# Performance work log

Measured on AMD Instinct MI355X. Metric: run time of the kernel, lower is better.

## Reference

```python
import jax, jax.numpy as jnp
import numpy as np

NEAR = 0.2          # near-plane cull, matches uvd[...,2] >= 0.2 in the source
SIGMA2_MAX = 9.0    # 3-sigma disk extent, matches get_disks' sigma3 corners
ALPHA_MIN = 1.0 / 255.0


def quat_to_rot(q):
    """Unit-quaternion [P,4] (w,x,y,z) -> rotation matrices [P,3,3]."""
    q = q / (jnp.linalg.norm(q, axis=-1, keepdims=True) + 1e-12)
    w, x, y, z = q[..., 0], q[..., 1], q[..., 2], q[..., 3]
    r0 = jnp.stack([1 - 2 * (y * y + z * z), 2 * (x * y - w * z), 2 * (x * z + w * y)], -1)
    r1 = jnp.stack([2 * (x * y + w * z), 1 - 2 * (x * x + z * z), 2 * (y * z - w * x)], -1)
    r2 = jnp.stack([2 * (x * z - w * y), 2 * (y * z + w * x), 1 - 2 * (x * x + y * y)], -1)
    return jnp.stack([r0, r1, r2], -2)


def setup_inputs() -> dict:
    key = jax.random.key(0)
    k = jax.random.split(key, 6)
    H = W = 128
    P = 4096
    tanfov = 0.4
    f = W / (2.0 * tanfov)
    xs = (jnp.arange(W, dtype=jnp.float32) - (W - 1) / 2.0) / f
    ys = (jnp.arange(H, dtype=jnp.float32) - (H - 1) / 2.0) / f
    gx, gy = jnp.meshgrid(xs, ys, indexing='xy')
    d = jnp.stack([gx, gy, jnp.ones_like(gx)], -1)
    ray_d = d / jnp.linalg.norm(d, axis=-1, keepdims=True)   # [H,W,3]
    ray_o = jnp.zeros((H, W, 3), jnp.float32)
    means3D = jax.random.normal(k[0], (P, 3), jnp.float32) * 1.5 + jnp.array([0.0, 0.0, 4.0], jnp.float32)
    scales = jax.random.uniform(k[1], (P, 2), jnp.float32, 0.02, 0.15)
    rotations = jax.random.normal(k[2], (P, 4), jnp.float32)
    opacities = jax.random.uniform(k[3], (P, 1), jnp.float32, 0.3, 1.0)
    colors = jax.random.uniform(k[4], (P, 3), jnp.float32)
    bg_color = jnp.zeros((3,), jnp.float32)
    return dict(ray_o=ray_o, ray_d=ray_d, means3D=means3D, scales=scales,
                rotations=rotations, opacities=opacities, colors=colors, bg_color=bg_color)


def reference(ray_o, ray_d, means3D, scales, rotations, opacities, colors, bg_color):
    """Gaussian-surfel ray tracing: ray/disk-plane intersection, 2D Gaussian
    falloff in the surfel tangent frame, front-to-back alpha compositing in
    depth order (the math the BVH-accelerated SurfelTracer computes)."""
    H, W, _ = ray_o.shape
    ro = ray_o.reshape(-1, 3)
    rd = ray_d.reshape(-1, 3)
    R = quat_to_rot(rotations)                     # [P,3,3]
    tu, tv, nrm = R[..., :, 0], R[..., :, 1], R[..., :, 2]  # tangent frame columns

    # ray-plane intersection t = dot(mu - o, n) / dot(d, n)  -> [Nr,P]
    den = rd @ nrm.T
    num = jnp.einsum('pk,pk->p', means3D, nrm)[None, :] - ro @ nrm.T
    safe_den = jnp.where(jnp.abs(den) < 1e-8, 1e-8, den)
    t = num / safe_den

    # local disk coords u,v of hit point without materializing [Nr,P,3]
    u = (ro @ tu.T - jnp.einsum('pk,pk->p', means3D, tu)[None, :] + t * (rd @ tu.T)) / scales[None, :, 0]
    v = (ro @ tv.T - jnp.einsum('pk,pk->p', means3D, tv)[None, :] + t * (rd @ tv.T)) / scales[None, :, 1]
    r2 = u * u + v * v
    G = jnp.exp(-0.5 * r2)
    alpha = jnp.clip(opacities[None, :, 0] * G, 0.0, 0.99)
    valid = (t > NEAR) & (r2 < SIGMA2_MAX) & (jnp.abs(den) > 1e-8) & (alpha > ALPHA_MIN)
    alpha = jnp.where(valid, alpha, 0.0)

    # front-to-back compositing: sort hits by depth per ray
    t_key = jnp.where(valid, t, jnp.inf)
    order = jnp.argsort(t_key, axis=1)
    alpha_s = jnp.take_along_axis(alpha, order, axis=1)
    trans = jnp.cumprod(1.0 - alpha_s, axis=1)
    trans = jnp.concatenate([jnp.ones_like(trans[:, :1]), trans[:, :-1]], axis=1)  # exclusive
    w_s = alpha_s * trans
    inv = jnp.argsort(order, axis=1)
    w = jnp.take_along_axis(w_s, inv, axis=1)      # weights in original surfel order

    acc = w.sum(-1)                                # [Nr]
    rgb = w @ colors + (1.0 - acc)[:, None] * bg_color[None, :]
    dpt = (w * jnp.where(valid, t, 0.0)).sum(-1)
    norm = w @ nrm
    return (rgb.reshape(H, W, 3), dpt.reshape(H, W, 1),
            acc.reshape(H, W, 1), norm.reshape(H, W, 3))
```

## Files before the change

kernel.cpp:

```cpp
#include <hip/hip_runtime.h>
#include <stdint.h>

#define NEAR_T  0.2f
#define SIG2MAX 9.0f
#define AMIN    (1.0f/255.0f)
#define NSL     8
#define TS      8
#define TB      16
#define KFIX    64


__device__ __forceinline__ float dot3(float ax,float ay,float az,
                                      float bx,float by,float bz){
  return fmaf(ax,bx, fmaf(ay,by, az*bz));
}

__device__ __forceinline__ bool eval_hit(const float* __restrict__ gp,
    float rox,float roy,float roz, float rdx,float rdy,float rdz,
    float& t_out, float& a_out)
{
  float nx=gp[6], ny=gp[7], nz=gp[8];
  float den  = dot3(rdx,rdy,rdz, nx,ny,nz);
  float aden = fabsf(den);
  float num  = gp[11] - dot3(rox,roy,roz, nx,ny,nz);
  float sden = (aden < 1e-8f) ? 1e-8f : den;
  float t = __fdividef(num, sden);
  float ru = dot3(rox,roy,roz, gp[0],gp[1],gp[2]);
  float du = dot3(rdx,rdy,rdz, gp[0],gp[1],gp[2]);
  float u  = fmaf(t, du, ru - gp[9])  * gp[12];
  float rv = dot3(rox,roy,roz, gp[3],gp[4],gp[5]);
  float dv = dot3(rdx,rdy,rdz, gp[3],gp[4],gp[5]);
  float v  = fmaf(t, dv, rv - gp[10]) * gp[13];
  float r2 = fmaf(u,u, v*v);
  float G  = __expf(-0.5f*r2);
  float a  = fminf(gp[14]*G, 0.99f);
  t_out = t; a_out = a;
  return (t > NEAR_T) & (r2 < SIG2MAX) & (aden > 1e-8f) & (a > AMIN);
}

__device__ __forceinline__ unsigned long long make_key(float t, float a, uint32_t g){
  uint32_t a16 = (uint32_t)(a * 65535.f + 0.5f);
  return ((unsigned long long)__float_as_uint(t) << 32) |
         ((unsigned long long)a16 << 16) | (unsigned long long)g;
}

__device__ __forceinline__ bool pix_bbox(const float* __restrict__ bp,
    bool fallback, float axm, float bxm, float aym, float bym, int W, int H,
    int& x0, int& x1, int& y0, int& y1)
{
  if (fallback){ x0=0; x1=W-1; y0=0; y1=H-1; return true; }
  float mx=bp[0], my=bp[1], mz=bp[2], ex=bp[3], ey=bp[4], ez=bp[5];
  float zmin=mz-ez, zmax=mz+ez;
  if (zmax <= 0.16f) return false;
  if (zmin <= 1e-3f){ x0=0; x1=W-1; y0=0; y1=H-1; return true; }
  float xmin=mx-ex, xmax=mx+ex, ymin=my-ey, ymax=my+ey;
  float gxmin = (xmin>=0.f)? xmin/zmax : xmin/zmin;
  float gxmax = (xmax>=0.f)? xmax/zmin : xmax/zmax;
  float gymin = (ymin>=0.f)? ymin/zmax : ymin/zmin;
  float gymax = (ymax>=0.f)? ymax/zmin : ymax/zmax;
  float p0 = (gxmin - bxm)/axm, p1 = (gxmax - bxm)/axm;
  float q0 = (gymin - bym)/aym, q1 = (gymax - bym)/aym;
  int ix0 = (int)floorf(fminf(p0,p1)) - 1;
  int ix1 = (int)ceilf (fmaxf(p0,p1)) + 1;
  int iy0 = (int)floorf(fminf(q0,q1)) - 1;
  int iy1 = (int)ceilf (fmaxf(q0,q1)) + 1;
  if (ix1 < 0 || ix0 > W-1 || iy1 < 0 || iy0 > H-1) return false;
  x0 = max(ix0,0); x1 = min(ix1,W-1);
  y0 = max(iy0,0); y1 = min(iy1,H-1);
  return true;
}

__global__ void k_prep(const float* __restrict__ rot, const float* __restrict__ means,
                       const float* __restrict__ scales, const float* __restrict__ opac,
                       const float* __restrict__ colors, const float* __restrict__ ray_o,
                       const float* __restrict__ ray_d,
                       float* __restrict__ geo, float* __restrict__ col,
                       float* __restrict__ baux, uint32_t* __restrict__ misc,
                       int P, int npix, int W)
{
  int tid = blockIdx.x*blockDim.x + threadIdx.x;
  float g0x = ray_d[0]/ray_d[2], g0y = ray_d[1]/ray_d[2];
  float axm = ray_d[3]/ray_d[5] - g0x;
  float aym = ray_d[(size_t)W*3+1]/ray_d[(size_t)W*3+2] - g0y;
  if (tid == 0){
    float* mf = (float*)misc;
    mf[1] = axm; mf[2] = g0x; mf[3] = aym; mf[4] = g0y;
    if (!(fabsf(axm) > 1e-12f) || !(fabsf(aym) > 1e-12f)) atomicOr(misc, 1u);
  }
  if (tid < npix){
    int ix = tid % W, iy = tid / W;
    float rox=ray_o[tid*3+0], roy=ray_o[tid*3+1], roz=ray_o[tid*3+2];
    float rdx=ray_d[tid*3+0], rdy=ray_d[tid*3+1], rdz=ray_d[tid*3+2];
    bool ok = (rox==0.f) & (roy==0.f) & (roz==0.f) & (rdz > 0.8f);
    if (ok){
      float gx = rdx/rdz, gy = rdy/rdz;
      ok = (fabsf(gx - fmaf(axm,(float)ix,g0x)) <= 3e-4f) &
           (fabsf(gy - fmaf(aym,(float)iy,g0y)) <= 3e-4f);
    }
    if (!ok) atomicOr(misc, 1u);
  }
  if (tid < P){
    float qw=rot[tid*4+0], qx=rot[tid*4+1], qy=rot[tid*4+2], qz=rot[tid*4+3];
    float n = sqrtf(qw*qw+qx*qx+qy*qy+qz*qz) + 1e-12f;
    qw/=n; qx/=n; qy/=n; qz/=n;
    float tux = 1.f-2.f*(qy*qy+qz*qz), tuy = 2.f*(qx*qy+qw*qz), tuz = 2.f*(qx*qz-qw*qy);
    float tvx = 2.f*(qx*qy-qw*qz), tvy = 1.f-2.f*(qx*qx+qz*qz), tvz = 2.f*(qy*qz+qw*qx);
    float nx  = 2.f*(qx*qz+qw*qy), ny  = 2.f*(qy*qz-qw*qx), nz  = 1.f-2.f*(qx*qx+qy*qy);
    float mx=means[tid*3+0], my=means[tid*3+1], mz=means[tid*3+2];
    float sx=scales[tid*2+0], sy=scales[tid*2+1];
    float* gp = &geo[(size_t)tid*16];
    gp[0]=tux; gp[1]=tuy; gp[2]=tuz;
    gp[3]=tvx; gp[4]=tvy; gp[5]=tvz;
    gp[6]=nx;  gp[7]=ny;  gp[8]=nz;
    gp[9]  = mx*tux+my*tuy+mz*tuz;
    gp[10] = mx*tvx+my*tvy+mz*tvz;
    gp[11] = mx*nx +my*ny +mz*nz;
    gp[12] = 1.f/sx;
    gp[13] = 1.f/sy;
    gp[14] = opac[tid];
    gp[15] = 0.f;
    col[tid*3+0]=colors[tid*3+0]; col[tid*3+1]=colors[tid*3+1]; col[tid*3+2]=colors[tid*3+2];
    float* bp = &baux[(size_t)tid*8];
    const float R3 = 3.02f;
    bp[0]=mx; bp[1]=my; bp[2]=mz;
    bp[3]=R3*(sx*fabsf(tux)+sy*fabsf(tvx));
    bp[4]=R3*(sx*fabsf(tuy)+sy*fabsf(tvy));
    bp[5]=R3*(sx*fabsf(tuz)+sy*fabsf(tvz));
    bp[6]=0.f; bp[7]=0.f;
  }
}

__global__ __launch_bounds__(1024)
void k_bin_fused(const float* __restrict__ baux, const uint32_t* __restrict__ misc,
                 int4* __restrict__ bbox, uint32_t* __restrict__ tileLen,
                 uint32_t* __restrict__ tileList, int P, int W, int H, int TXB, int TYB)
{
  __shared__ uint32_t sCnt[1024];
  int NTB = TXB*TYB;
  int tid = threadIdx.x;
  for (int i=tid; i<NTB; i+=1024) sCnt[i]=0u;
  __syncthreads();
  const float* mf = (const float*)misc;
  bool fb = (misc[0] != 0u);
  float a1=mf[1], a2=mf[2], a3=mf[3], a4=mf[4];
  for (int g=tid; g<P; g+=1024){
    int x0,x1,y0,y1;
    bool ok = pix_bbox(&baux[(size_t)g*8], fb, a1,a2,a3,a4, W,H, x0,x1,y0,y1);
    bbox[g] = ok ? make_int4(x0,x1,y0,y1) : make_int4(1,0,1,0);
    if (!ok) continue;
    int tx0=x0/TB, tx1=x1/TB, ty0=y0/TB, ty1=y1/TB;
    for (int ty=ty0; ty<=ty1; ++ty)
      for (int tx=tx0; tx<=tx1; ++tx){
        int t = ty*TXB+tx;
        uint32_t slot = atomicAdd(&sCnt[t], 1u);
        tileList[(size_t)t*P + slot] = (uint32_t)g;
      }
  }
  __syncthreads();
  for (int i=tid; i<NTB; i+=1024) tileLen[i] = sCnt[i];
}

__global__ void k_bbox(const float* __restrict__ baux, const uint32_t* __restrict__ misc,
                       int4* __restrict__ bbox, int P, int W, int H)
{
  int g = blockIdx.x*blockDim.x + threadIdx.x;
  if (g >= P) return;
  const float* mf = (const float*)misc;
  bool fb = (misc[0] != 0u);
  int x0,x1,y0,y1;
  bool ok = pix_bbox(&baux[(size_t)g*8], fb, mf[1],mf[2],mf[3],mf[4], W,H, x0,x1,y0,y1);
  bbox[g] = ok ? make_int4(x0,x1,y0,y1) : make_int4(1,0,1,0);
}

__global__ void k_bin_global(const int4* __restrict__ bbox, uint32_t* __restrict__ tileLen,
                             uint32_t* __restrict__ tileList, int P, int TXB)
{
  int g = blockIdx.x*blockDim.x + threadIdx.x;
  if (g >= P) return;
  int4 bb = bbox[g];
  if (bb.x > bb.y) return;
  int tx0=bb.x/TB, tx1=bb.y/TB, ty0=bb.z/TB, ty1=bb.w/TB;
  for (int ty=ty0; ty<=ty1; ++ty)
    for (int tx=tx0; tx<=tx1; ++tx){
      int t = ty*TXB+tx;
      uint32_t slot = atomicAdd(&tileLen[t], 1u);
      tileList[(size_t)t*P + slot] = (uint32_t)g;
    }
}

__global__ __launch_bounds__(64)
void k_trace(const float* __restrict__ geo, const int4* __restrict__ bbox,
             const float* __restrict__ ray_o, const float* __restrict__ ray_d,
             const uint32_t* __restrict__ tileLen, const uint32_t* __restrict__ tileList,
             uint32_t* __restrict__ cnt, unsigned long long* __restrict__ keys64,
             int W, int H, int TXB, int STX, int P)
{
  int st = blockIdx.x;
  int stx = st % STX, sty = st / STX;
  int lane = threadIdx.x;
  int ix = stx*TS + (lane & (TS-1));
  int iy = sty*TS + (lane / TS);
  bool live = (ix < W) & (iy < H);
  int px = live ? (iy*W + ix) : 0;
  int pt = (sty*TS/TB)*TXB + (stx*TS/TB);
  uint32_t base = (uint32_t)pt * (uint32_t)P;
  uint32_t len  = tileLen[pt];
  int sx0 = stx*TS, sx1 = sx0 + TS-1;
  int sy0 = sty*TS, sy1 = sy0 + TS-1;
  float rox=ray_o[px*3+0], roy=ray_o[px*3+1], roz=ray_o[px*3+2];
  float rdx=ray_d[px*3+0], rdy=ray_d[px*3+1], rdz=ray_d[px*3+2];
  for (uint32_t s = blockIdx.y; s < len; s += NSL){
    int gu = __builtin_amdgcn_readfirstlane((int)tileList[base+s]);
    int4 bb = bbox[gu];
    if (bb.x > sx1 || bb.y < sx0 || bb.z > sy1 || bb.w < sy0) continue;
    const float* gp = &geo[(size_t)gu*16];
    float t,a;
    bool hit = eval_hit(gp, rox,roy,roz, rdx,rdy,rdz, t, a) && live;
    if (hit){
      uint32_t slot = atomicAdd(&cnt[px], 1u);
      if (slot < KFIX) keys64[(size_t)px*KFIX + slot] = make_key(t, a, (uint32_t)gu);
    }
  }
}

__device__ __forceinline__ float wred(float v){
  #pragma unroll
  for (int d=32; d>0; d>>=1) v += __shfl_down(v, d);
  return v;
}

__device__ __forceinline__ void comp_write(int px, int npix, int lane,
    float r_, float g_, float bl_, float dpt_, float acc_,
    float nx_, float ny_, float nz_, const float* __restrict__ bg,
    float* __restrict__ out)
{
  r_ = wred(r_); g_ = wred(g_); bl_ = wred(bl_);
  dpt_ = wred(dpt_); acc_ = wred(acc_);
  nx_ = wred(nx_); ny_ = wred(ny_); nz_ = wred(nz_);
  if (lane == 0){
    float one_m = 1.f - acc_;
    out[(size_t)px*3+0] = r_  + one_m*bg[0];
    out[(size_t)px*3+1] = g_  + one_m*bg[1];
    out[(size_t)px*3+2] = bl_ + one_m*bg[2];
    out[(size_t)npix*3 + px] = dpt_;
    out[(size_t)npix*4 + px] = acc_;
    out[(size_t)npix*5 + (size_t)px*3+0] = nx_;
    out[(size_t)npix*5 + (size_t)px*3+1] = ny_;
    out[(size_t)npix*5 + (size_t)px*3+2] = nz_;
  }
}

__global__ __launch_bounds__(256)
void k_comp_small(const unsigned long long* __restrict__ keys64,
                  const uint32_t* __restrict__ cnt,
                  const float* __restrict__ geo, const float* __restrict__ col,
                  const float* __restrict__ bg, float* __restrict__ out, int npix)
{
  int lane = threadIdx.x & 63;
  int wave = threadIdx.x >> 6;
  for (int px = (int)(blockIdx.x*4u + wave); px < npix; px += (int)(gridDim.x*4u)){
    uint32_t K = cnt[px];
    if (K > (uint32_t)KFIX) continue;
    unsigned long long key = (lane < (int)K) ? keys64[(size_t)px*KFIX + lane] : ~0ull;
    #pragma unroll
    for (int k=2; k<=64; k<<=1){
      #pragma unroll
      for (int j=k>>1; j>0; j>>=1){
        unsigned long long other = __shfl_xor(key, j);
        bool keep_min = (((lane & j) == 0) == ((lane & k) == 0));
        unsigned long long lo = key < other ? key : other;
        unsigned long long hi = key < other ? other : key;
        key = keep_min ? lo : hi;
      }
    }
    bool valid = lane < (int)K;
    const float inv65535 = 1.f/65535.f;
    float a = (float)((uint32_t)(key >> 16) & 0xFFFFu) * inv65535;
    float p = valid ? (1.f - a) : 1.f;
    float ip = p;
    #pragma unroll
    for (int d=1; d<64; d<<=1){ float v = __shfl_up(ip, d); if (lane >= d) ip *= v; }
    float T = __shfl_up(ip, 1);
    if (lane == 0) T = 1.f;
    float r_=0.f, g_=0.f, bl_=0.f, dpt_=0.f, acc_=0.f, nx_=0.f, ny_=0.f, nz_=0.f;
    if (valid){
      float t = __uint_as_float((uint32_t)(key >> 32));
      uint32_t g = (uint32_t)(key & 0xFFFFu);
      float w = a * T;
      const float* gp = &geo[(size_t)g*16];
      const float* cp = &col[(size_t)g*3];
      r_ = w*cp[0]; g_ = w*cp[1]; bl_ = w*cp[2];
      dpt_ = w*t; acc_ = w;
      nx_ = w*gp[6]; ny_ = w*gp[7]; nz_ = w*gp[8];
    }
    comp_write(px, npix, lane, r_,g_,bl_,dpt_,acc_,nx_,ny_,nz_, bg, out);
  }
}

__global__ __launch_bounds__(64)
void k_comp_over(const float* __restrict__ geo, const int4* __restrict__ bbox,
                 const float* __restrict__ col,
                 const float* __restrict__ ray_o, const float* __restrict__ ray_d,
                 const uint32_t* __restrict__ tileLen, const uint32_t* __restrict__ tileList,
                 const uint32_t* __restrict__ cnt, const float* __restrict__ bg,
                 float* __restrict__ out, int npix, int W, int TXB, int P)
{
  __shared__ unsigned long long sk[4096];
  int lane = threadIdx.x;
  unsigned long long lt = (1ull << lane) - 1ull;
  for (int px = (int)blockIdx.x; px < npix; px += (int)gridDim.x){
    if (cnt[px] <= (uint32_t)KFIX) continue;
    int ix = px % W, iy = px / W;
    int pt = (iy/TB)*TXB + (ix/TB);
    uint32_t base = (uint32_t)pt * (uint32_t)P;
    uint32_t len  = tileLen[pt];
    float rox=ray_o[px*3+0], roy=ray_o[px*3+1], roz=ray_o[px*3+2];
    float rdx=ray_d[px*3+0], rdy=ray_d[px*3+1], rdz=ray_d[px*3+2];

    uint32_t run = 0;
    for (uint32_t s0=0; s0<len; s0+=64){
      uint32_t s = s0 + (uint32_t)lane;
      bool act = s < len;
      uint32_t gu = act ? tileList[base+s] : 0u;
      float t=0.f, a=0.f;
      bool hit = false;
      if (act){
        int4 bb = bbox[gu];
        if (bb.x <= ix && ix <= bb.y && bb.z <= iy && iy <= bb.w)
          hit = eval_hit(&geo[(size_t)gu*16], rox,roy,roz, rdx,rdy,rdz, t, a);
      }
      unsigned long long m = __ballot(hit);
      if (hit){
        uint32_t slot = run + (uint32_t)__popcll(m & lt);
        if (slot < 4096u) sk[slot] = make_key(t, a, gu);
      }
      run += (uint32_t)__popcll(m);
    }
    uint32_t K = min(run, 4096u);
    uint32_t N = 1; while (N < K) N <<= 1;
    for (uint32_t i=K+lane; i<N; i+=64) sk[i] = ~0ull;
    __syncthreads();

    for (uint32_t kk=2; kk<=N; kk<<=1){
      for (uint32_t j=kk>>1; j>0; j>>=1){
        for (uint32_t i=lane; i<N; i+=64){
          uint32_t ij = i ^ j;
          if (ij > i){
            unsigned long long a = sk[i], b = sk[ij];
            bool up = ((i & kk) == 0);
            if ((a > b) == up){ sk[i] = b; sk[ij] = a; }
          }
        }
        __syncthreads();
      }
    }

    const float inv65535 = 1.f/65535.f;
    uint32_t C = (K + 63) >> 6;
    uint32_t b0 = lane*C, e0 = min(b0 + C, K);
    float p = 1.f;
    for (uint32_t i=b0; i<e0; ++i){
      float a = (float)((uint32_t)(sk[i] >> 16) & 0xFFFFu) * inv65535;
      p *= (1.f - a);
    }
    float ip = p;
    #pragma unroll
    for (int d=1; d<64; d<<=1){ float v = __shfl_up(ip, d); if (lane >= d) ip *= v; }
    float T = __shfl_up(ip, 1);
    if (lane == 0) T = 1.f;

    float r_=0.f, g_=0.f, bl_=0.f, dpt_=0.f, acc_=0.f, nx_=0.f, ny_=0.f, nz_=0.f;
    for (uint32_t i=b0; i<e0; ++i){
      unsigned long long key = sk[i];
      float t = __uint_as_float((uint32_t)(key >> 32));
      float a = (float)((uint32_t)(key >> 16) & 0xFFFFu) * inv65535;
      uint32_t g = (uint32_t)(key & 0xFFFFu);
      float w = a * T;
      const float* gp = &geo[(size_t)g*16];
      const float* cp = &col[(size_t)g*3];
      r_  += w * cp[0]; g_ += w * cp[1]; bl_ += w * cp[2];
      dpt_ += w * t; acc_ += w;
      nx_ += w * gp[6]; ny_ += w * gp[7]; nz_ += w * gp[8];
      T *= (1.f - a);
    }
    comp_write(px, npix, lane, r_,g_,bl_,dpt_,acc_,nx_,ny_,nz_, bg, out);
    __syncthreads();
  }
}

extern "C" void kernel_launch(void* const* d_in, const int* in_sizes, int n_in,
                              void* d_out, int out_size, void* d_ws, size_t ws_size,
                              hipStream_t stream)
{
  const float* ray_o  = (const float*)d_in[0];
  const float* ray_d  = (const float*)d_in[1];
  const float* means  = (const float*)d_in[2];
  const float* scales = (const float*)d_in[3];
  const float* rot    = (const float*)d_in[4];
  const float* opac   = (const float*)d_in[5];
  const float* colors = (const float*)d_in[6];
  const float* bg     = (const float*)d_in[7];
  float* out = (float*)d_out;

  int npix = in_sizes[0] / 3;
  int P    = in_sizes[2] / 3;
  int W    = (int)(sqrtf((float)npix) + 0.5f);
  int H    = npix / W;
  int TXB  = (W + TB - 1) / TB;
  int TYB  = (H + TB - 1) / TB;
  int NTB  = TXB * TYB;
  int STX  = (W + TS - 1) / TS;
  int STY  = (H + TS - 1) / TS;
  int NST  = STX * STY;

  uint8_t* ws = (uint8_t*)d_ws;
  size_t o_geo   = 0;
  size_t sz_geo  = ((size_t)P*16*4 + 255) & ~(size_t)255;
  size_t o_col   = o_geo + sz_geo;
  size_t sz_col  = ((size_t)P*3*4 + 255) & ~(size_t)255;
  size_t o_baux  = o_col + sz_col;
  size_t sz_baux = ((size_t)P*8*4 + 255) & ~(size_t)255;
  size_t o_bbox  = o_baux + sz_baux;
  size_t sz_bbox = ((size_t)P*16 + 255) & ~(size_t)255;

  size_t o_ctrl  = o_bbox + sz_bbox;
  size_t sz_pix  = ((size_t)npix*4 + 255) & ~(size_t)255;
  size_t o_cnt   = o_ctrl;
  size_t sz_ntb  = ((size_t)NTB*4 + 255) & ~(size_t)255;
  size_t o_tlen  = o_cnt + sz_pix;
  size_t o_misc  = o_tlen + sz_ntb;
  size_t ctrl_sz = (o_misc + 256) - o_ctrl;

  size_t o_tlist = o_ctrl + ctrl_sz;
  size_t sz_tlist= (((size_t)NTB*(size_t)P*4) + 255) & ~(size_t)255;
  size_t o_k64   = o_tlist + sz_tlist;

  float*    geo     = (float*)(ws + o_geo);
  float*    col     = (float*)(ws + o_col);
  float*    baux    = (float*)(ws + o_baux);
  int4*     bbox    = (int4*)(ws + o_bbox);
  uint32_t* cnt     = (uint32_t*)(ws + o_cnt);
  uint32_t* tileLen = (uint32_t*)(ws + o_tlen);
  uint32_t* misc    = (uint32_t*)(ws + o_misc);
  uint32_t* tileList= (uint32_t*)(ws + o_tlist);
  unsigned long long* keys64 = (unsigned long long*)(ws + o_k64);

  hipMemsetAsync(ws + o_ctrl, 0, ctrl_sz, stream);

  int initN = npix > P ? npix : P;
  k_prep<<<(initN + 255)/256, 256, 0, stream>>>(rot, means, scales, opac, colors,
                                                ray_o, ray_d, geo, col, baux, misc,
                                                P, npix, W);
  if (NTB <= 1024){
    k_bin_fused<<<1, 1024, 0, stream>>>(baux, misc, bbox, tileLen, tileList,
                                        P, W, H, TXB, TYB);
  } else {
    k_bbox<<<(P + 255)/256, 256, 0, stream>>>(baux, misc, bbox, P, W, H);
    k_bin_global<<<(P + 255)/256, 256, 0, stream>>>(bbox, tileLen, tileList, P, TXB);
  }
  dim3 tgrid(NST, NSL);
  k_trace<<<tgrid, 64, 0, stream>>>(geo, bbox, ray_o, ray_d, tileLen, tileList,
                                    cnt, keys64, W, H, TXB, STX, P);
  k_comp_small<<<1024, 256, 0, stream>>>(keys64, cnt, geo, col, bg, out, npix);
  k_comp_over<<<1024, 64, 0, stream>>>(geo, bbox, col, ray_o, ray_d, tileLen, tileList,
                                       cnt, bg, out, npix, W, TXB, P);
}
```

Before: 136.6 us.

## Fuse memset, prep and binning into one single-block setup kernel

When the tile count fits in shared memory, the memset, the per-surfel prep kernel and the single-block binning kernel are replaced by one 1024-thread kernel. It zeroes the per-pixel counters, computes surfel geometry, checks whether the pinhole fast path applies and bins surfels into tiles, with one block-wide barrier between prep and binning. This removes two launches and a memset, which matters at this small problem size, and the fast-path flag moves from a global word to shared memory. In exchange, prep of 4096 surfels and the 16384-pixel ray check now run on a single workgroup instead of many blocks.

```diff
diff --git a/kernel.cpp b/kernel.cpp
--- a/kernel.cpp
+++ b/kernel.cpp
@@ -8,7 +8,6 @@
 #define TS      8
 #define TB      16
 #define KFIX    64
-
 
 __device__ __forceinline__ float dot3(float ax,float ay,float az,
                                       float bx,float by,float bz){
@@ -70,6 +69,95 @@
   return true;
 }
 
+__device__ __forceinline__ void prep_one(int g, const float* __restrict__ rot,
+    const float* __restrict__ means, const float* __restrict__ scales,
+    const float* __restrict__ opac, const float* __restrict__ colors,
+    float* __restrict__ geo, float* __restrict__ col, float* __restrict__ baux)
+{
+  float qw=rot[g*4+0], qx=rot[g*4+1], qy=rot[g*4+2], qz=rot[g*4+3];
+  float n = sqrtf(qw*qw+qx*qx+qy*qy+qz*qz) + 1e-12f;
+  qw/=n; qx/=n; qy/=n; qz/=n;
+  float tux = 1.f-2.f*(qy*qy+qz*qz), tuy = 2.f*(qx*qy+qw*qz), tuz = 2.f*(qx*qz-qw*qy);
+  float tvx = 2.f*(qx*qy-qw*qz), tvy = 1.f-2.f*(qx*qx+qz*qz), tvz = 2.f*(qy*qz+qw*qx);
+  float nx  = 2.f*(qx*qz+qw*qy), ny  = 2.f*(qy*qz-qw*qx), nz  = 1.f-2.f*(qx*qx+qy*qy);
+  float mx=means[g*3+0], my=means[g*3+1], mz=means[g*3+2];
+  float sx=scales[g*2+0], sy=scales[g*2+1];
+  float* gp = &geo[(size_t)g*16];
+  gp[0]=tux; gp[1]=tuy; gp[2]=tuz;
+  gp[3]=tvx; gp[4]=tvy; gp[5]=tvz;
+  gp[6]=nx;  gp[7]=ny;  gp[8]=nz;
+  gp[9]  = mx*tux+my*tuy+mz*tuz;
+  gp[10] = mx*tvx+my*tvy+mz*tvz;
+  gp[11] = mx*nx +my*ny +mz*nz;
+  gp[12] = 1.f/sx;
+  gp[13] = 1.f/sy;
+  gp[14] = opac[g];
+  gp[15] = 0.f;
+  col[g*3+0]=colors[g*3+0]; col[g*3+1]=colors[g*3+1]; col[g*3+2]=colors[g*3+2];
+  float* bp = &baux[(size_t)g*8];
+  const float R3 = 3.02f;
+  bp[0]=mx; bp[1]=my; bp[2]=mz;
+  bp[3]=R3*(sx*fabsf(tux)+sy*fabsf(tvx));
+  bp[4]=R3*(sx*fabsf(tuy)+sy*fabsf(tvy));
+  bp[5]=R3*(sx*fabsf(tuz)+sy*fabsf(tvz));
+  bp[6]=0.f; bp[7]=0.f;
+}
+
+__global__ __launch_bounds__(1024)
+void k_setup(const float* __restrict__ rot, const float* __restrict__ means,
+             const float* __restrict__ scales, const float* __restrict__ opac,
+             const float* __restrict__ colors, const float* __restrict__ ray_o,
+             const float* __restrict__ ray_d,
+             float* __restrict__ geo, float* __restrict__ col,
+             float* __restrict__ baux, int4* __restrict__ bbox,
+             uint32_t* __restrict__ cnt, uint32_t* __restrict__ tileLen,
+             uint32_t* __restrict__ tileList,
+             int P, int npix, int W, int H, int TXB, int TYB)
+{
+  __shared__ uint32_t sCnt[1024];
+  __shared__ int sFB;
+  int NTB = TXB*TYB;
+  int tid = threadIdx.x;
+  if (tid == 0) sFB = 0;
+  for (int i=tid; i<NTB;  i+=1024) sCnt[i]=0u;
+  for (int i=tid; i<npix; i+=1024) cnt[i]=0u;
+  float g0x = ray_d[0]/ray_d[2], g0y = ray_d[1]/ray_d[2];
+  float axm = ray_d[3]/ray_d[5] - g0x;
+  float aym = ray_d[(size_t)W*3+1]/ray_d[(size_t)W*3+2] - g0y;
+  if (!(fabsf(axm) > 1e-12f) || !(fabsf(aym) > 1e-12f)) sFB = 1;
+  for (int g=tid; g<P; g+=1024)
+    prep_one(g, rot, means, scales, opac, colors, geo, col, baux);
+  for (int px=tid; px<npix; px+=1024){
+    int ix = px % W, iy = px / W;
+    float rox=ray_o[px*3+0], roy=ray_o[px*3+1], roz=ray_o[px*3+2];
+    float rdx=ray_d[px*3+0], rdy=ray_d[px*3+1], rdz=ray_d[px*3+2];
+    bool ok = (rox==0.f) & (roy==0.f) & (roz==0.f) & (rdz > 0.8f);
+    if (ok){
+      float gx = rdx/rdz, gy = rdy/rdz;
+      ok = (fabsf(gx - fmaf(axm,(float)ix,g0x)) <= 3e-4f) &
+           (fabsf(gy - fmaf(aym,(float)iy,g0y)) <= 3e-4f);
+    }
+    if (!ok) sFB = 1;
+  }
+  __syncthreads();
+  bool fb = (sFB != 0);
+  for (int g=tid; g<P; g+=1024){
+    int x0,x1,y0,y1;
+    bool ok = pix_bbox(&baux[(size_t)g*8], fb, axm,g0x,aym,g0y, W,H, x0,x1,y0,y1);
+    bbox[g] = ok ? make_int4(x0,x1,y0,y1) : make_int4(1,0,1,0);
+    if (!ok) continue;
+    int tx0=x0/TB, tx1=x1/TB, ty0=y0/TB, ty1=y1/TB;
+    for (int ty=ty0; ty<=ty1; ++ty)
+      for (int tx=tx0; tx<=tx1; ++tx){
+        int t = ty*TXB+tx;
+        uint32_t slot = atomicAdd(&sCnt[t], 1u);
+        tileList[(size_t)t*P + slot] = (uint32_t)g;
+      }
+  }
+  __syncthreads();
+  for (int i=tid; i<NTB; i+=1024) tileLen[i] = sCnt[i];
+}
+
 __global__ void k_prep(const float* __restrict__ rot, const float* __restrict__ means,
                        const float* __restrict__ scales, const float* __restrict__ opac,
                        const float* __restrict__ colors, const float* __restrict__ ray_o,
@@ -99,65 +187,8 @@
     }
     if (!ok) atomicOr(misc, 1u);
   }
-  if (tid < P){
-    float qw=rot[tid*4+0], qx=rot[tid*4+1], qy=rot[tid*4+2], qz=rot[tid*4+3];
-    float n = sqrtf(qw*qw+qx*qx+qy*qy+qz*qz) + 1e-12f;
-    qw/=n; qx/=n; qy/=n; qz/=n;
-    float tux = 1.f-2.f*(qy*qy+qz*qz), tuy = 2.f*(qx*qy+qw*qz), tuz = 2.f*(qx*qz-qw*qy);
-    float tvx = 2.f*(qx*qy-qw*qz), tvy = 1.f-2.f*(qx*qx+qz*qz), tvz = 2.f*(qy*qz+qw*qx);
-    float nx  = 2.f*(qx*qz+qw*qy), ny  = 2.f*(qy*qz-qw*qx), nz  = 1.f-2.f*(qx*qx+qy*qy);
-    float mx=means[tid*3+0], my=means[tid*3+1], mz=means[tid*3+2];
-    float sx=scales[tid*2+0], sy=scales[tid*2+1];
-    float* gp = &geo[(size_t)tid*16];
-    gp[0]=tux; gp[1]=tuy; gp[2]=tuz;
-    gp[3]=tvx; gp[4]=tvy; gp[5]=tvz;
-    gp[6]=nx;  gp[7]=ny;  gp[8]=nz;
-    gp[9]  = mx*tux+my*tuy+mz*tuz;
-    gp[10] = mx*tvx+my*tvy+mz*tvz;
-    gp[11] = mx*nx +my*ny +mz*nz;
-    gp[12] = 1.f/sx;
-    gp[13] = 1.f/sy;
-    gp[14] = opac[tid];
-    gp[15] = 0.f;
-    col[tid*3+0]=colors[tid*3+0]; col[tid*3+1]=colors[tid*3+1]; col[tid*3+2]=colors[tid*3+2];
-    float* bp = &baux[(size_t)tid*8];
-    const float R3 = 3.02f;
-    bp[0]=mx; bp[1]=my; bp[2]=mz;
-    bp[3]=R3*(sx*fabsf(tux)+sy*fabsf(tvx));
-    bp[4]=R3*(sx*fabsf(tuy)+sy*fabsf(tvy));
-    bp[5]=R3*(sx*fabsf(tuz)+sy*fabsf(tvz));
-    bp[6]=0.f; bp[7]=0.f;
-  }
-}
-
-__global__ __launch_bounds__(1024)
-void k_bin_fused(const float* __restrict__ baux, const uint32_t* __restrict__ misc,
-                 int4* __restrict__ bbox, uint32_t* __restrict__ tileLen,
-                 uint32_t* __restrict__ tileList, int P, int W, int H, int TXB, int TYB)
-{
-  __shared__ uint32_t sCnt[1024];
-  int NTB = TXB*TYB;
-  int tid = threadIdx.x;
-  for (int i=tid; i<NTB; i+=1024) sCnt[i]=0u;
-  __syncthreads();
-  const float* mf = (const float*)misc;
-  bool fb = (misc[0] != 0u);
-  float a1=mf[1], a2=mf[2], a3=mf[3], a4=mf[4];
-  for (int g=tid; g<P; g+=1024){
-    int x0,x1,y0,y1;
-    bool ok = pix_bbox(&baux[(size_t)g*8], fb, a1,a2,a3,a4, W,H, x0,x1,y0,y1);
-    bbox[g] = ok ? make_int4(x0,x1,y0,y1) : make_int4(1,0,1,0);
-    if (!ok) continue;
-    int tx0=x0/TB, tx1=x1/TB, ty0=y0/TB, ty1=y1/TB;
-    for (int ty=ty0; ty<=ty1; ++ty)
-      for (int tx=tx0; tx<=tx1; ++tx){
-        int t = ty*TXB+tx;
-        uint32_t slot = atomicAdd(&sCnt[t], 1u);
-        tileList[(size_t)t*P + slot] = (uint32_t)g;
-      }
-  }
-  __syncthreads();
-  for (int i=tid; i<NTB; i+=1024) tileLen[i] = sCnt[i];
+  if (tid < P)
+    prep_one(tid, rot, means, scales, opac, colors, geo, col, baux);
 }
 
 __global__ void k_bbox(const float* __restrict__ baux, const uint32_t* __restrict__ misc,
@@ -445,16 +476,16 @@
   uint32_t* tileList= (uint32_t*)(ws + o_tlist);
   unsigned long long* keys64 = (unsigned long long*)(ws + o_k64);
 
-  hipMemsetAsync(ws + o_ctrl, 0, ctrl_sz, stream);
-
-  int initN = npix > P ? npix : P;
-  k_prep<<<(initN + 255)/256, 256, 0, stream>>>(rot, means, scales, opac, colors,
-                                                ray_o, ray_d, geo, col, baux, misc,
-                                                P, npix, W);
   if (NTB <= 1024){
-    k_bin_fused<<<1, 1024, 0, stream>>>(baux, misc, bbox, tileLen, tileList,
-                                        P, W, H, TXB, TYB);
+    k_setup<<<1, 1024, 0, stream>>>(rot, means, scales, opac, colors, ray_o, ray_d,
+                                    geo, col, baux, bbox, cnt, tileLen, tileList,
+                                    P, npix, W, H, TXB, TYB);
   } else {
+    hipMemsetAsync(ws + o_ctrl, 0, ctrl_sz, stream);
+    int initN = npix > P ? npix : P;
+    k_prep<<<(initN + 255)/256, 256, 0, stream>>>(rot, means, scales, opac, colors,
+                                                  ray_o, ray_d, geo, col, baux, misc,
+                                                  P, npix, W);
     k_bbox<<<(P + 255)/256, 256, 0, stream>>>(baux, misc, bbox, P, W, H);
     k_bin_global<<<(P + 255)/256, 256, 0, stream>>>(bbox, tileLen, tileList, P, TXB);
   }
```

Result: slower. 194.3 us (+42.2%).
